# Optimization experiments

Measured on AMD Instinct MI355X. Metric: run time of the kernel, lower is better.

Reference implementation:

```python
import jax, jax.numpy as jnp
import numpy as np

B, DIN, D = 1000, 1024, 512
C, L = 1203, 77
N_INS, N_EX = 4, 5
K_SEL, K_TOP = 32, 5
HEADS, DH, MLP, NL = 8, 64, 2048, 4
TEMP = 50.0


def setup_inputs() -> dict:
    key = jax.random.key(0)
    ks = iter(jax.random.split(key, 64))

    def rn(shape, s=0.02):
        return jax.random.normal(next(ks), shape, dtype=jnp.float32) * s

    def layer_params(prefix):
        return {
            prefix + '_ln1_g': jnp.ones((NL, D)), prefix + '_ln1_b': jnp.zeros((NL, D)),
            prefix + '_qkv_w': rn((NL, D, 3 * D)), prefix + '_qkv_b': jnp.zeros((NL, 3 * D)),
            prefix + '_out_w': rn((NL, D, D)), prefix + '_out_b': jnp.zeros((NL, D)),
            prefix + '_ln2_g': jnp.ones((NL, D)), prefix + '_ln2_b': jnp.zeros((NL, D)),
            prefix + '_fc_w': rn((NL, D, MLP)), prefix + '_fc_b': jnp.zeros((NL, MLP)),
            prefix + '_pr_w': rn((NL, MLP, D)), prefix + '_pr_b': jnp.zeros((NL, D)),
        }

    zw = jax.random.normal(next(ks), (D, C + 1), dtype=jnp.float32)
    zw = zw / jnp.linalg.norm(zw, axis=0, keepdims=True)  # F.normalize(dim=0) as in __init__
    inp = {
        'x': jax.random.normal(next(ks), (B, DIN), dtype=jnp.float32),
        'linear_w': rn((DIN, D)), 'linear_b': jnp.zeros((D,)),
        'zs_weight': zw,
        'sample_w': rn((D, D)), 'sample_b': jnp.zeros((D,)),
        'ins_token': rn((N_INS, D), 0.1),
        'token_seq': rn((C, L, D), 0.1),
        'exemplar': rn((C, N_EX, D), 0.1),
        'eos_index': jax.random.randint(next(ks), (C,), 5, 60, dtype=jnp.int32),
    }
    inp.update(layer_params('agg'))
    inp['pos_emb'] = rn((L, D), 0.01)
    inp.update(layer_params('txt'))
    inp['lnf_g'] = jnp.ones((D,))
    inp['lnf_b'] = jnp.zeros((D,))
    inp['text_proj'] = rn((D, D))
    return inp


def layernorm(x, g, b, eps=1e-5):
    m = x.mean(-1, keepdims=True)
    v = x.var(-1, keepdims=True)
    return (x - m) * jax.lax.rsqrt(v + eps) * g + b


def quick_gelu(x):  # CLIP QuickGELU
    return x * jax.nn.sigmoid(1.702 * x)


def transformer(h, ln1g, ln1b, qkvw, qkvb, ow, ob, ln2g, ln2b, fcw, fcb, prw, prb, mask=None):
    # h: [N, S, D]; pre-LN residual attention blocks (CLIP style)
    Bn, S, _ = h.shape
    scale = np.float32(1.0 / np.sqrt(DH))
    for i in range(NL):
        a = layernorm(h, ln1g[i], ln1b[i])
        qkv = a @ qkvw[i] + qkvb[i]
        q, k, v = jnp.split(qkv, 3, axis=-1)
        q = q.reshape(Bn, S, HEADS, DH)
        k = k.reshape(Bn, S, HEADS, DH)
        v = v.reshape(Bn, S, HEADS, DH)
        s = jnp.einsum('bqhd,bkhd->bhqk', q, k) * scale
        if mask is not None:
            s = s + mask
        o = jnp.einsum('bhqk,bkhd->bqhd', jax.nn.softmax(s, axis=-1), v).reshape(Bn, S, D)
        h = h + o @ ow[i] + ob[i]
        m = layernorm(h, ln2g[i], ln2b[i])
        h = h + quick_gelu(m @ fcw[i] + fcb[i]) @ prw[i] + prb[i]
    return h


def inverse_sigmoid(x, eps=1e-5):
    x = jnp.clip(x, 0.0, 1.0)
    x1 = jnp.clip(x, eps, None)
    x2 = jnp.clip(1.0 - x, eps, None)
    return jnp.log(x1 / x2)


def reference(x, linear_w, linear_b, zs_weight, sample_w, sample_b, ins_token, token_seq,
              exemplar, eos_index,
              agg_ln1_g, agg_ln1_b, agg_qkv_w, agg_qkv_b, agg_out_w, agg_out_b,
              agg_ln2_g, agg_ln2_b, agg_fc_w, agg_fc_b, agg_pr_w, agg_pr_b,
              pos_emb, txt_ln1_g, txt_ln1_b, txt_qkv_w, txt_qkv_b, txt_out_w, txt_out_b,
              txt_ln2_g, txt_ln2_b, txt_fc_w, txt_fc_b, txt_pr_w, txt_pr_b,
              lnf_g, lnf_b, text_proj):
    # ---- base classifier ----
    h = x @ linear_w + linear_b                                        # [B, D]
    h = TEMP * h / jnp.linalg.norm(h, axis=1, keepdims=True)
    logits = h @ zs_weight                                             # [B, C+1]
    # ---- entropy-based proposal selection (eval path, k=32) ----
    p = jax.nn.sigmoid(logits)
    entropy = (-p * jax.nn.log_sigmoid(logits)).sum(-1)                # [B]
    _, select_index = jax.lax.top_k(entropy, K_SEL)                    # [32]
    sel_logits = logits[select_index]                                  # [32, C+1]
    _, topk_index = jax.lax.top_k(sel_logits[:, :-1], K_TOP)           # [32, 5]
    sampled_x = jax.lax.stop_gradient(h[select_index]) @ sample_w + sample_b  # [32, D]
    # ---- batched aggregator input (replaces per-proposal python loop) ----
    base = ins_token[None] + (sampled_x / TEMP)[:, None, :]            # [32, N_INS, D]
    base = jnp.broadcast_to(base[:, None], (K_SEL, K_TOP, N_INS, D))
    ex = exemplar[topk_index]                                          # [32, 5, N_EX, D]
    agg_in = jnp.concatenate([base, ex], axis=2).reshape(K_SEL * K_TOP, N_INS + N_EX, D)
    agg_out = transformer(agg_in, agg_ln1_g, agg_ln1_b, agg_qkv_w, agg_qkv_b, agg_out_w,
                          agg_out_b, agg_ln2_g, agg_ln2_b, agg_fc_w, agg_fc_b, agg_pr_w, agg_pr_b)
    ins_tokens = agg_out[:, :N_INS].reshape(K_SEL, K_TOP, N_INS, D)
    # ---- splice instance tokens into class prompts ----
    prompt = token_seq[topk_index]                                     # [32, 5, L, D]
    upd = jnp.concatenate([prompt[:, :, :2], ins_tokens, prompt[:, :, 2:L - N_INS]], axis=2)
    # ---- CLIP text encoder on updated prompts ----
    t = upd.reshape(K_SEL * K_TOP, L, D) + pos_emb
    causal = jnp.where(jnp.tril(jnp.ones((L, L), bool)), 0.0, -1e9).astype(jnp.float32)
    t = transformer(t, txt_ln1_g, txt_ln1_b, txt_qkv_w, txt_qkv_b, txt_out_w, txt_out_b,
                    txt_ln2_g, txt_ln2_b, txt_fc_w, txt_fc_b, txt_pr_w, txt_pr_b, mask=causal)
    t = layernorm(t, lnf_g, lnf_b)
    eos = (eos_index[topk_index] + 2 * N_INS).reshape(-1)              # [160]
    feats = t[jnp.arange(K_SEL * K_TOP), eos] @ text_proj              # [160, D]
    feats = feats / jnp.linalg.norm(feats, axis=-1, keepdims=True)
    rerank_logits = jnp.einsum('sd,skd->sk', sampled_x, feats.reshape(K_SEL, K_TOP, D))
    # ---- fuse + scatter back ----
    sel_det = jax.lax.stop_gradient(sel_logits)
    sel_topk = jnp.take_along_axis(sel_det, topk_index, axis=1)
    fused = jax.nn.sigmoid(sel_topk) ** 0.75 * jax.nn.sigmoid(rerank_logits) ** 0.25
    reranked = inverse_sigmoid(fused)
    rows = jnp.arange(K_SEL)[:, None]
    logits_clone = sel_det.at[rows, topk_index].set(reranked)
    logits_final = logits.at[select_index].set(logits_clone)
    return logits, rerank_logits, select_index, logits_final
```

## Files before the change

kernel.cpp:

```cpp
#include <hip/hip_runtime.h>
#include <math.h>

#define TID ((int)threadIdx.x)

constexpr int Bsz = 1000, DIN = 1024, Dm = 512, C1 = 1204, C0 = 1203, Ltok = 77;
constexpr int NINS = 4, NEX = 5, KSEL = 32, KTOP = 5, NHEAD = 8, DH = 64, MLPD = 2048, NL = 4, Pn = 160;
constexpr float TEMPc = 50.0f;

typedef __attribute__((ext_vector_type(8))) short short8;
typedef __attribute__((ext_vector_type(4))) float f32x4;
typedef __attribute__((address_space(1))) const void g1void;
typedef __attribute__((address_space(3))) void l3void;
#define GLOAD16(g, l) __builtin_amdgcn_global_load_lds((g1void*)(g), (l3void*)(l), 16, 0, 0)

__device__ __forceinline__ float sigf(float z) {
  return z >= 0.f ? 1.f / (1.f + expf(-z)) : expf(z) / (1.f + expf(z));
}

__device__ __forceinline__ float qgelu(float v) {
  return v * __fdividef(1.f, 1.f + __expf(-1.702f * v));
}

__device__ __forceinline__ unsigned short f2bfu(float f) {
  unsigned u = __builtin_bit_cast(unsigned, f);
  u += 0x7fffu + ((u >> 16) & 1u);
  return (unsigned short)(u >> 16);
}
__device__ __forceinline__ short f2bf(float f) { return (short)f2bfu(f); }

__device__ __forceinline__ void epi_store(f32x4 v, const float* bias, int colb, size_t off,
                                          int mode, float* Cf, short* Cb, float* Xres) {
  if (bias) {
    float4 bv = *(const float4*)(bias + colb);
    v[0] += bv.x; v[1] += bv.y; v[2] += bv.z; v[3] += bv.w;
  }
  if (mode == 0) {
    *(float4*)(Cf + off) = make_float4(v[0], v[1], v[2], v[3]);
  } else if (mode == 1) {
    float4* p = (float4*)(Xres + off);
    float4 o = *p;
    o.x += v[0]; o.y += v[1]; o.z += v[2]; o.w += v[3];
    *p = o;
  } else {
    if (mode == 2) {
      v[0] = qgelu(v[0]); v[1] = qgelu(v[1]); v[2] = qgelu(v[2]); v[3] = qgelu(v[3]);
    }
    uint2 pk;
    pk.x = (unsigned)f2bfu(v[0]) | ((unsigned)f2bfu(v[1]) << 16);
    pk.y = (unsigned)f2bfu(v[2]) | ((unsigned)f2bfu(v[3]) << 16);
    *(uint2*)(Cb + off) = pk;
  }
}

__global__ __launch_bounds__(256, 4) void bgemm_k(const short* __restrict__ A,
                                                  const short* __restrict__ Bt,
                                                  const float* __restrict__ bias,
                                                  float* __restrict__ Cf,
                                                  short* __restrict__ Cb,
                                                  float* __restrict__ Xres,
                                                  int M, int N, int K, int mode) {
  __shared__ short As[8192];
  __shared__ short Bs[8192];
  int nwg = gridDim.x * gridDim.y;
  int orig = blockIdx.y * gridDim.x + blockIdx.x;
  int xcd = orig & 7, lid = orig >> 3;
  int q = nwg >> 3, r = nwg & 7;
  int swz = (xcd < r ? xcd * (q + 1) : r * (q + 1) + (xcd - r) * q) + lid;
  int row0 = (swz / gridDim.x) * 128, col0 = (swz % gridDim.x) * 128;
  int lane = TID & 63;
  int w = TID >> 6;
  int wr = (TID >> 7) & 1, wc = (TID >> 6) & 1;
  int skb = (TID >> 4) & 3, si = TID & 15;
  f32x4 acc[4][4] = {};
  int nt = K >> 6;
  int kb = lane >> 4, i = lane & 15;
  for (int t = 0; t < nt; ++t) {
#pragma unroll
    for (int s = 0; s < 2; ++s) {
#pragma unroll
      for (int c = 0; c < 2; ++c) {
        int row = (c * 4 + w) * 16 + si;
        int k0 = (t << 6) + (s << 5) + skb * 8;
        GLOAD16(A + (size_t)(row0 + row) * K + k0, As + s * 4096 + (c * 256 + w * 64) * 8);
        GLOAD16(Bt + (size_t)(col0 + row) * K + k0, Bs + s * 4096 + (c * 256 + w * 64) * 8);
      }
    }
    __syncthreads();
#pragma unroll
    for (int s = 0; s < 2; ++s) {
      const short* Ab = As + s * 4096;
      const short* Bb = Bs + s * 4096;
      short8 af[4], bfr[4];
#pragma unroll
      for (int m = 0; m < 4; ++m)
        af[m] = *(const short8*)(Ab + ((((wr * 4 + m) * 4 + kb) * 16 + i) * 8));
#pragma unroll
      for (int n = 0; n < 4; ++n)
        bfr[n] = *(const short8*)(Bb + ((((wc * 4 + n) * 4 + kb) * 16 + i) * 8));
#pragma unroll
      for (int m = 0; m < 4; ++m)
#pragma unroll
        for (int n = 0; n < 4; ++n)
          acc[m][n] = __builtin_amdgcn_mfma_f32_16x16x32_bf16(bfr[n], af[m], acc[m][n], 0, 0, 0);
    }
    __syncthreads();
  }
  int li = lane & 15, lg = lane >> 4;
#pragma unroll
  for (int m = 0; m < 4; ++m) {
    int row = row0 + wr * 64 + m * 16 + li;
    if (row >= M) continue;
#pragma unroll
    for (int n = 0; n < 4; ++n) {
      int colb = col0 + wc * 64 + n * 16 + lg * 4;
      epi_store(acc[m][n], bias, colb, (size_t)row * N + colb, mode, Cf, Cb, Xres);
    }
  }
}

__global__ __launch_bounds__(512, 4) void bgemm_tall_k(const short* __restrict__ A,
                                                       const short* __restrict__ Bt,
                                                       const float* __restrict__ bias,
                                                       float* __restrict__ Cf,
                                                       short* __restrict__ Cb,
                                                       float* __restrict__ Xres,
                                                       int M, int N, int K, int mode) {
  __shared__ short As[16384];
  __shared__ short Bs[8192];
  int nwg = gridDim.x * gridDim.y;
  int orig = blockIdx.y * gridDim.x + blockIdx.x;
  int xcd = orig & 7, lid = orig >> 3;
  int q = nwg >> 3, r = nwg & 7;
  int swz = (xcd < r ? xcd * (q + 1) : r * (q + 1) + (xcd - r) * q) + lid;
  int row0 = (swz / gridDim.x) * 256, col0 = (swz % gridDim.x) * 128;
  int lane = TID & 63;
  int w = TID >> 6;
  int wr = w >> 1, wc = w & 1;
  f32x4 acc[4][4] = {};
  int nt = K >> 6;
  int kb = lane >> 4, i = lane & 15;
  int sg0 = TID >> 6, skb = (TID >> 4) & 3, si = TID & 15;
  for (int t = 0; t < nt; ++t) {
#pragma unroll
    for (int s = 0; s < 2; ++s) {
      int k0 = (t << 6) + (s << 5) + skb * 8;
#pragma unroll
      for (int c0 = 0; c0 < 2; ++c0) {
        int row = (c0 * 8 + sg0) * 16 + si;
        GLOAD16(A + (size_t)(row0 + row) * K + k0, As + s * 8192 + (c0 * 512 + TID) * 8);
      }
      {
        int row = sg0 * 16 + si;
        GLOAD16(Bt + (size_t)(col0 + row) * K + k0, Bs + s * 4096 + TID * 8);
      }
    }
    __syncthreads();
#pragma unroll
    for (int s = 0; s < 2; ++s) {
      const short* Ab = As + s * 8192;
      const short* Bb = Bs + s * 4096;
      short8 af[4], bfr[4];
#pragma unroll
      for (int m = 0; m < 4; ++m)
        af[m] = *(const short8*)(Ab + ((((wr * 4 + m) * 4 + kb) * 16 + i) * 8));
#pragma unroll
      for (int n = 0; n < 4; ++n)
        bfr[n] = *(const short8*)(Bb + ((((wc * 4 + n) * 4 + kb) * 16 + i) * 8));
#pragma unroll
      for (int m = 0; m < 4; ++m)
#pragma unroll
        for (int n = 0; n < 4; ++n)
          acc[m][n] = __builtin_amdgcn_mfma_f32_16x16x32_bf16(bfr[n], af[m], acc[m][n], 0, 0, 0);
    }
    __syncthreads();
  }
  int li = lane & 15, lg = lane >> 4;
#pragma unroll
  for (int m = 0; m < 4; ++m) {
    int row = row0 + wr * 64 + m * 16 + li;
    if (row >= M) continue;
#pragma unroll
    for (int n = 0; n < 4; ++n) {
      int colb = col0 + wc * 64 + n * 16 + lg * 4;
      epi_store(acc[m][n], bias, colb, (size_t)row * N + colb, mode, Cf, Cb, Xres);
    }
  }
}

__global__ __launch_bounds__(256) void wconv_k(const float* __restrict__ W,
                                               short* __restrict__ Wt, int K, int N) {
  int l = blockIdx.z;
  const float* Wl = W + (size_t)l * K * N;
  short* Wtl = Wt + (size_t)l * K * N;
  __shared__ float t[32][33];
  int n0 = blockIdx.x * 32, k0 = blockIdx.y * 32;
  int tx = TID & 31, ty = TID >> 5;
#pragma unroll
  for (int u = 0; u < 4; ++u)
    t[ty + u * 8][tx] = Wl[(size_t)(k0 + ty + u * 8) * N + n0 + tx];
  __syncthreads();
#pragma unroll
  for (int u = 0; u < 4; ++u)
    Wtl[(size_t)(n0 + ty + u * 8) * K + k0 + tx] = f2bf(t[tx][ty + u * 8]);
}

__global__ __launch_bounds__(256) void gemm32s_k(const float* __restrict__ A,
                                                 const float* __restrict__ W,
                                                 float* __restrict__ P,
                                                 int M, int N, int K, int KC) {
  __shared__ float As[64][17];
  __shared__ float Ws[16][65];
  int tx = TID & 15, ty = TID >> 4;
  int row0 = blockIdx.y * 64, col0 = blockIdx.x * 64;
  int kbeg = blockIdx.z * KC;
  int kend = kbeg + KC < K ? kbeg + KC : K;
  float acc[4][4] = {};
  for (int k0 = kbeg; k0 < kend; k0 += 16) {
    {
      int r = TID >> 2, c4 = (TID & 3) * 4;
      int gr = row0 + r;
#pragma unroll
      for (int u = 0; u < 4; ++u) {
        int gc = k0 + c4 + u;
        As[r][c4 + u] = (gr < M && gc < K) ? A[gr * K + gc] : 0.f;
      }
    }
    {
      int c = TID & 63;
      int gc = col0 + c;
#pragma unroll
      for (int u = 0; u < 4; ++u) {
        int rr = (TID >> 6) * 4 + u;
        int gk = k0 + rr;
        Ws[rr][c] = (gk < K && gc < N) ? W[gk * N + gc] : 0.f;
      }
    }
    __syncthreads();
#pragma unroll
    for (int kk = 0; kk < 16; ++kk) {
      float a[4], b[4];
#pragma unroll
      for (int i = 0; i < 4; ++i) a[i] = As[ty * 4 + i][kk];
#pragma unroll
      for (int j = 0; j < 4; ++j) b[j] = Ws[kk][tx * 4 + j];
#pragma unroll
      for (int i = 0; i < 4; ++i)
#pragma unroll
        for (int j = 0; j < 4; ++j) acc[i][j] += a[i] * b[j];
    }
    __syncthreads();
  }
  float* Ps = P + (size_t)blockIdx.z * M * N;
#pragma unroll
  for (int i = 0; i < 4; ++i) {
    int rrow = row0 + ty * 4 + i;
    if (rrow >= M) continue;
#pragma unroll
    for (int j = 0; j < 4; ++j) {
      int ccol = col0 + tx * 4 + j;
      if (ccol >= N) continue;
      Ps[(size_t)rrow * N + ccol] = acc[i][j];
    }
  }
}

__global__ __launch_bounds__(256) void reduce_k(const float* __restrict__ P,
                                                const float* __restrict__ bias,
                                                float* __restrict__ C,
                                                float* __restrict__ C2,
                                                int MN, int N, int S) {
  int i = blockIdx.x * 256 + TID;
  if (i >= MN) return;
  float v = 0.f;
  for (int s = 0; s < S; ++s) v += P[(size_t)s * MN + i];
  if (bias) v += bias[i % N];
  C[i] = v;
  if (C2) C2[i] = v;
}

__global__ __launch_bounds__(256) void rownorm_k(float* __restrict__ h) {
  int r = blockIdx.x;
  float* x = h + r * Dm;
  float v0 = x[TID], v1 = x[TID + 256];
  __shared__ float s1[256];
  s1[TID] = v0 * v0 + v1 * v1;
  __syncthreads();
  for (int s = 128; s; s >>= 1) { if (TID < s) s1[TID] += s1[TID + s]; __syncthreads(); }
  float sc = TEMPc / sqrtf(s1[0]);
  x[TID] = v0 * sc;
  x[TID + 256] = v1 * sc;
}

__global__ __launch_bounds__(256) void entropy_k(const float* __restrict__ logits,
                                                 double* __restrict__ ent) {
  int r = blockIdx.x;
  double acc = 0.0;
  for (int c = TID; c < C1; c += 256) {
    float z = logits[r * C1 + c];
    float ls = z >= 0.f ? -log1pf(expf(-z)) : z - log1pf(expf(z));
    float p = z >= 0.f ? 1.f / (1.f + expf(-z)) : expf(z) / (1.f + expf(z));
    acc += (double)(-p * ls);
  }
  __shared__ double sd[256];
  sd[TID] = acc;
  __syncthreads();
  for (int s = 128; s; s >>= 1) { if (TID < s) sd[TID] += sd[TID + s]; __syncthreads(); }
  if (TID == 0) ent[r] = sd[0];
}

__global__ __launch_bounds__(256) void top32_k(const double* __restrict__ ent,
                                               int* __restrict__ selidx,
                                               float* __restrict__ out2) {
  __shared__ double v[1000];
  __shared__ double wv[4];
  __shared__ int wi[4];
  for (int i = TID; i < 1000; i += 256) v[i] = ent[i];
  __syncthreads();
  int w = TID >> 6, lane = TID & 63;
  for (int r = 0; r < KSEL; ++r) {
    double bv = -1e300; int bi = 1 << 30;
    for (int i = TID; i < 1000; i += 256) {
      double x = v[i];
      if (x > bv || (x == bv && i < bi)) { bv = x; bi = i; }
    }
#pragma unroll
    for (int off = 32; off; off >>= 1) {
      double ov = __shfl_xor(bv, off, 64);
      int oi = __shfl_xor(bi, off, 64);
      if (ov > bv || (ov == bv && oi < bi)) { bv = ov; bi = oi; }
    }
    if (lane == 0) { wv[w] = bv; wi[w] = bi; }
    __syncthreads();
    if (TID == 0) {
      double fv = wv[0]; int fi = wi[0];
#pragma unroll
      for (int u = 1; u < 4; ++u)
        if (wv[u] > fv || (wv[u] == fv && wi[u] < fi)) { fv = wv[u]; fi = wi[u]; }
      selidx[r] = fi; out2[r] = (float)fi; v[fi] = -1e300;
    }
    __syncthreads();
  }
}

__global__ __launch_bounds__(256) void top5_k(const float* __restrict__ logits,
                                              const int* __restrict__ selidx,
                                              int* __restrict__ topk) {
  int s = blockIdx.x;
  int row = selidx[s];
  __shared__ float v[C0];
  __shared__ float wv[4];
  __shared__ int wi[4];
  for (int i = TID; i < C0; i += 256) v[i] = logits[row * C1 + i];
  __syncthreads();
  int w = TID >> 6, lane = TID & 63;
  for (int r = 0; r < KTOP; ++r) {
    float bv = -INFINITY; int bi = 1 << 30;
    for (int i = TID; i < C0; i += 256) {
      float x = v[i];
      if (x > bv || (x == bv && i < bi)) { bv = x; bi = i; }
    }
#pragma unroll
    for (int off = 32; off; off >>= 1) {
      float ov = __shfl_xor(bv, off, 64);
      int oi = __shfl_xor(bi, off, 64);
      if (ov > bv || (ov == bv && oi < bi)) { bv = ov; bi = oi; }
    }
    if (lane == 0) { wv[w] = bv; wi[w] = bi; }
    __syncthreads();
    if (TID == 0) {
      float fv = wv[0]; int fi = wi[0];
#pragma unroll
      for (int u = 1; u < 4; ++u)
        if (wv[u] > fv || (wv[u] == fv && wi[u] < fi)) { fv = wv[u]; fi = wi[u]; }
      topk[s * KTOP + r] = fi; v[fi] = -INFINITY;
    }
    __syncthreads();
  }
}

__global__ void eos_k(const int* __restrict__ eos_index, const int* __restrict__ topk,
                      int* __restrict__ eosl) {
  for (int p = TID; p < Pn; p += 256) eosl[p] = eos_index[topk[p]] + 2 * NINS;
}

__global__ void gather_h_k(const float* __restrict__ h, const int* __restrict__ selidx,
                           float* __restrict__ hsel) {
  int s = blockIdx.x;
  int row = selidx[s];
  for (int d = TID; d < Dm; d += 256) hsel[s * Dm + d] = h[row * Dm + d];
}

__global__ __launch_bounds__(256) void build_agg_k(const float* __restrict__ ins,
                                                   const float* __restrict__ sampled,
                                                   const float* __restrict__ ex,
                                                   const int* __restrict__ topk,
                                                   float* __restrict__ X) {
  int b = blockIdx.x;
  int p = b / 9, tok = b % 9;
  int s = p / KTOP;
#pragma unroll
  for (int u = 0; u < 2; ++u) {
    int d = TID + u * 256;
    float v;
    if (tok < NINS) v = ins[tok * Dm + d] + sampled[s * Dm + d] * (1.f / TEMPc);
    else {
      int cls = topk[p];
      v = ex[(cls * NEX + (tok - NINS)) * Dm + d];
    }
    X[b * Dm + d] = v;
  }
}

__global__ void save_ins_k(const float* __restrict__ X, float* __restrict__ insbuf) {
  int p = blockIdx.x;
  for (int i = TID; i < NINS * Dm; i += 256) insbuf[p * NINS * Dm + i] = X[p * 9 * Dm + i];
}

__global__ __launch_bounds__(256) void build_txt_k(const float* __restrict__ token_seq,
                                                   const float* __restrict__ insbuf,
                                                   const float* __restrict__ pos,
                                                   const int* __restrict__ topk,
                                                   float* __restrict__ X, int p0) {
  int b = blockIdx.x;
  int pl = b / Ltok, tok = b % Ltok;
  int p = p0 + pl;
  int cls = topk[p];
#pragma unroll
  for (int u = 0; u < 2; ++u) {
    int d = TID + u * 256;
    float v;
    if (tok < 2) v = token_seq[(cls * Ltok + tok) * Dm + d];
    else if (tok < 2 + NINS) v = insbuf[(p * NINS + (tok - 2)) * Dm + d];
    else v = token_seq[(cls * Ltok + (tok - NINS)) * Dm + d];
    X[b * Dm + d] = v + pos[tok * Dm + d];
  }
}

__global__ __launch_bounds__(256) void ln_k(const float* __restrict__ X,
                                            const float* __restrict__ g,
                                            const float* __restrict__ b,
                                            short* __restrict__ A) {
  int t = blockIdx.x;
  const float* x = X + t * Dm;
  float v0 = x[TID], v1 = x[TID + 256];
  __shared__ float s1[256], s2[256];
  s1[TID] = v0 + v1;
  s2[TID] = v0 * v0 + v1 * v1;
  __syncthreads();
  for (int s = 128; s; s >>= 1) {
    if (TID < s) { s1[TID] += s1[TID + s]; s2[TID] += s2[TID + s]; }
    __syncthreads();
  }
  float mean = s1[0] * (1.f / 512.f);
  float var = s2[0] * (1.f / 512.f) - mean * mean;
  float inv = rsqrtf(var + 1e-5f);
  A[t * Dm + TID] = f2bf((v0 - mean) * inv * g[TID] + b[TID]);
  A[t * Dm + TID + 256] = f2bf((v1 - mean) * inv * g[TID + 256] + b[TID + 256]);
}

__global__ __launch_bounds__(320) void attn_tx_k(const short* __restrict__ qkv,
                                                 short* __restrict__ O, int S) {
  __shared__ short Kf[5120];
  __shared__ short Vt[6144];
  __shared__ short Pf[5][1536];
  int p = blockIdx.x >> 3, h = blockIdx.x & 7;
  int base = p * S;
  for (int c = TID; c < 640; c += 320) {
    int i = c & 15, kb = (c >> 4) & 7, g = c >> 7;
    int j = g * 16 + i;
    short8 v = {};
    if (j < S) v = *(const short8*)(qkv + (size_t)(base + j) * 1536 + 512 + h * 64 + kb * 8);
    *(short8*)(Kf + c * 8) = v;
  }
  for (int c = TID; c < 640; c += 320) {
    int j = c >> 3;
    int d0 = (c & 7) * 8;
    short8 v = {};
    if (j < S) v = *(const short8*)(qkv + (size_t)(base + j) * 1536 + 1024 + h * 64 + d0);
    int kb = j >> 3, jj = j & 7;
#pragma unroll
    for (int u = 0; u < 8; ++u) {
      int d = d0 + u;
      Vt[(((d >> 4) * 12 + kb) * 16 + (d & 15)) * 8 + jj] = v[u];
    }
  }
  for (int c = TID; c < 128; c += 320) {
    int i = c & 15, kb = 10 + ((c >> 4) & 1), g = c >> 5;
    *(short8*)(Vt + ((g * 12 + kb) * 16 + i) * 8) = short8{};
  }
  __syncthreads();
  int w = TID >> 6, lane = TID & 63;
  int li = lane & 15, lg = lane >> 4;
  short8 aq[2];
#pragma unroll
  for (int ks = 0; ks < 2; ++ks)
    aq[ks] = *(const short8*)(qkv + (size_t)(base + w * 16 + li) * 1536 + h * 64 + ks * 32 + lg * 8);
  f32x4 accs[5] = {};
#pragma unroll
  for (int t = 0; t < 5; ++t)
#pragma unroll
    for (int ks = 0; ks < 2; ++ks) {
      short8 bk = *(const short8*)(Kf + ((t * 8 + ks * 4 + lg) * 16 + li) * 8);
      accs[t] = __builtin_amdgcn_mfma_f32_16x16x32_bf16(aq[ks], bk, accs[t], 0, 0, 0);
    }
  int rowg = w * 16 + lg * 4;
#pragma unroll
  for (int r = 0; r < 4; ++r) {
    int row = rowg + r;
    float v[5];
    float mx = -1e30f;
#pragma unroll
    for (int t = 0; t < 5; ++t) {
      int col = t * 16 + li;
      float x = accs[t][r] * 0.125f;
      bool ok = (col < S) && (col <= row);
      v[t] = ok ? x : -1e30f;
      mx = fmaxf(mx, v[t]);
    }
#pragma unroll
    for (int off = 1; off < 16; off <<= 1) mx = fmaxf(mx, __shfl_xor(mx, off, 64));
    float sum = 0.f;
#pragma unroll
    for (int t = 0; t < 5; ++t) {
      v[t] = (v[t] > -1e29f) ? __expf(v[t] - mx) : 0.f;
      sum += v[t];
    }
#pragma unroll
    for (int off = 1; off < 16; off <<= 1) sum += __shfl_xor(sum, off, 64);
    float inv = __fdividef(1.f, sum);
#pragma unroll
    for (int t = 0; t < 5; ++t) {
      int c = t * 16 + li;
      Pf[w][((c >> 3) * 16 + (row - w * 16)) * 8 + (c & 7)] = f2bf(v[t] * inv);
    }
  }
  for (int z = lane; z < 256; z += 64) {
    int kb = 10 + (z >> 7);
    int rem = z & 127;
    Pf[w][(kb * 16 + (rem >> 3)) * 8 + (rem & 7)] = 0;
  }
  f32x4 acco[4] = {};
#pragma unroll
  for (int s = 0; s < 3; ++s) {
    short8 ap = *(const short8*)(Pf[w] + ((s * 4 + lg) * 16 + li) * 8);
#pragma unroll
    for (int n = 0; n < 4; ++n) {
      short8 bv = *(const short8*)(Vt + ((n * 12 + s * 4 + lg) * 16 + li) * 8);
      acco[n] = __builtin_amdgcn_mfma_f32_16x16x32_bf16(ap, bv, acco[n], 0, 0, 0);
    }
  }
#pragma unroll
  for (int n = 0; n < 4; ++n)
#pragma unroll
    for (int r = 0; r < 4; ++r) {
      int row = rowg + r;
      if (row < S) O[(size_t)(base + row) * 512 + h * 64 + n * 16 + li] = f2bf(acco[n][r]);
    }
}

__global__ __launch_bounds__(256) void attn_k(const float* __restrict__ qkv,
                                              short* __restrict__ O, int S, int causal) {
  int blk = blockIdx.x;
  int p = blk >> 3, h = blk & 7;
  __shared__ float Qs[Ltok][68], Ks[Ltok][68], Vs[Ltok][68];
  __shared__ float ps[4][132];
  int base = p * S;
  for (int idx = TID; idx < S * 16; idx += 256) {
    int j = idx >> 4, c = idx & 15;
    const float4* q = (const float4*)(qkv + (size_t)(base + j) * 1536 + h * 64);
    const float4* k = (const float4*)(qkv + (size_t)(base + j) * 1536 + 512 + h * 64);
    const float4* v = (const float4*)(qkv + (size_t)(base + j) * 1536 + 1024 + h * 64);
    ((float4*)&Qs[j][0])[c] = q[c];
    ((float4*)&Ks[j][0])[c] = k[c];
    ((float4*)&Vs[j][0])[c] = v[c];
  }
  __syncthreads();
  int wave = TID >> 6, lane = TID & 63;
  bool val0 = lane < S, val1 = lane + 64 < S;
  int j0 = val0 ? lane : 0;
  int j1 = val1 ? lane + 64 : 0;
  const float4* k0p = (const float4*)&Ks[j0][0];
  const float4* k1p = (const float4*)&Ks[j1][0];
  for (int i = wave; i < S; i += 4) {
    const float4* q4 = (const float4*)&Qs[i][0];
    float a0 = 0.f, a1 = 0.f;
#pragma unroll
    for (int d4 = 0; d4 < 16; ++d4) {
      float4 qv = q4[d4], k0v = k0p[d4], k1v = k1p[d4];
      a0 += qv.x * k0v.x + qv.y * k0v.y + qv.z * k0v.z + qv.w * k0v.w;
      a1 += qv.x * k1v.x + qv.y * k1v.y + qv.z * k1v.z + qv.w * k1v.w;
    }
    float m0 = (val0 && (!causal || lane <= i)) ? a0 * 0.125f : -1e30f;
    float m1 = (val1 && (!causal || lane + 64 <= i)) ? a1 * 0.125f : -1e30f;
    float mx = fmaxf(m0, m1);
#pragma unroll
    for (int off = 32; off; off >>= 1) mx = fmaxf(mx, __shfl_xor(mx, off, 64));
    float e0 = expf(m0 - mx), e1 = expf(m1 - mx);
    float sum = e0 + e1;
#pragma unroll
    for (int off = 32; off; off >>= 1) sum += __shfl_xor(sum, off, 64);
    float inv = 1.f / sum;
    ps[wave][lane] = e0 * inv;
    ps[wave][lane + 64] = e1 * inv;
    float o = 0.f;
    for (int j = 0; j < S; ++j) o += ps[wave][j] * Vs[j][lane];
    O[(base + i) * Dm + h * 64 + lane] = f2bf(o);
  }
}

__global__ __launch_bounds__(256) void feats_k(const float* __restrict__ X,
                                               const int* __restrict__ eosl,
                                               const float* __restrict__ g,
                                               const float* __restrict__ bb,
                                               const float* __restrict__ proj,
                                               float* __restrict__ feats, int p0) {
  int pl = blockIdx.x;
  int p = p0 + pl;
  int e = eosl[p];
  const float* x = X + (size_t)(pl * Ltok + e) * Dm;
  __shared__ float row[Dm];
  __shared__ float s1[256], s2[256];
  float v0 = x[TID], v1 = x[TID + 256];
  s1[TID] = v0 + v1;
  s2[TID] = v0 * v0 + v1 * v1;
  __syncthreads();
  for (int s = 128; s; s >>= 1) {
    if (TID < s) { s1[TID] += s1[TID + s]; s2[TID] += s2[TID + s]; }
    __syncthreads();
  }
  float mean = s1[0] * (1.f / 512.f);
  float var = s2[0] * (1.f / 512.f) - mean * mean;
  float inv = rsqrtf(var + 1e-5f);
  row[TID] = (v0 - mean) * inv * g[TID] + bb[TID];
  row[TID + 256] = (v1 - mean) * inv * g[TID + 256] + bb[TID + 256];
  __syncthreads();
  float a0 = 0.f, a1 = 0.f;
  for (int d = 0; d < Dm; ++d) {
    float r = row[d];
    a0 += r * proj[d * Dm + TID];
    a1 += r * proj[d * Dm + TID + 256];
  }
  s1[TID] = a0 * a0 + a1 * a1;
  __syncthreads();
  for (int s = 128; s; s >>= 1) { if (TID < s) s1[TID] += s1[TID + s]; __syncthreads(); }
  float sc = 1.f / sqrtf(s1[0]);
  feats[p * Dm + TID] = a0 * sc;
  feats[p * Dm + TID + 256] = a1 * sc;
}

__global__ void rerank_k(const float* __restrict__ sampled, const float* __restrict__ feats,
                         const int* __restrict__ selidx, const int* __restrict__ topk,
                         const float* __restrict__ logits, float* __restrict__ out1,
                         float* __restrict__ out3) {
  int idx = blockIdx.x;
  int s = idx / KTOP;
  int lane = TID;
  float acc = 0.f;
  for (int d = lane; d < Dm; d += 64) acc += sampled[s * Dm + d] * feats[idx * Dm + d];
#pragma unroll
  for (int off = 32; off; off >>= 1) acc += __shfl_down(acc, off, 64);
  if (lane == 0) {
    out1[idx] = acc;
    int row = selidx[s];
    int cls = topk[idx];
    float sl = logits[row * C1 + cls];
    float a = sigf(sl), b = sigf(acc);
    float fused = powf(a, 0.75f) * powf(b, 0.25f);
    float xx = fminf(fmaxf(fused, 0.f), 1.f);
    float x1 = fmaxf(xx, 1e-5f);
    float x2 = fmaxf(1.f - xx, 1e-5f);
    out3[row * C1 + cls] = logf(x1 / x2);
  }
}

static inline size_t alup(size_t x) { return (x + 255) & ~(size_t)255; }

constexpr size_t WT_QKV = (size_t)NL * Dm * 3 * Dm;
constexpr size_t WT_OUT = (size_t)NL * Dm * Dm;
constexpr size_t WT_FC  = (size_t)NL * Dm * MLPD;
constexpr size_t WT_PR  = (size_t)NL * MLPD * Dm;
constexpr size_t WT_ALL = WT_QKV + WT_OUT + WT_FC + WT_PR;

static void plan_rows(int PC, size_t* rows_o, size_t* RP_o) {
  size_t rows = (size_t)PC * Ltok;
  if (rows < (size_t)(Pn * 9)) rows = Pn * 9;
  size_t RP = (rows + 255) & ~(size_t)255;
  *rows_o = rows; *RP_o = RP;
}

static size_t plan_bytes(int PC) {
  size_t rows, RP;
  plan_rows(PC, &rows, &RP);
  size_t tot = 0;
  tot += alup(Bsz * Dm * 4);
  tot += alup(Bsz * 8);
  tot += alup(KSEL * 4);
  tot += alup(Pn * 4);
  tot += alup(Pn * 4);
  tot += alup(KSEL * Dm * 4);
  tot += alup(KSEL * Dm * 4);
  tot += alup(Pn * NINS * Dm * 4);
  tot += alup(Pn * Dm * 4);
  tot += alup(rows * Dm * 4);
  tot += alup(RP * Dm * 2);
  tot += alup(RP * Dm * 2);
  tot += alup((size_t)(Pn * 9) * 3 * Dm * 4);
  tot += alup(RP * 3 * Dm * 2);
  tot += alup(RP * MLPD * 2);
  tot += 2 * alup(WT_ALL * 2);
  tot += alup((size_t)8 * Bsz * Dm * 4);
  tot += alup((size_t)4 * Bsz * C1 * 4);
  tot += alup((size_t)8 * KSEL * Dm * 4);
  return tot;
}

extern "C" void kernel_launch(void* const* d_in, const int* in_sizes, int n_in,
                              void* d_out, int out_size, void* d_ws, size_t ws_size,
                              hipStream_t stream) {
  const float* x         = (const float*)d_in[0];
  const float* linear_w  = (const float*)d_in[1];
  const float* linear_b  = (const float*)d_in[2];
  const float* zs_w      = (const float*)d_in[3];
  const float* sample_w  = (const float*)d_in[4];
  const float* sample_b  = (const float*)d_in[5];
  const float* ins_token = (const float*)d_in[6];
  const float* token_seq = (const float*)d_in[7];
  const float* exemplar  = (const float*)d_in[8];
  const int*   eos_index = (const int*)d_in[9];
  const float* agg_ln1_g = (const float*)d_in[10];
  const float* agg_ln1_b = (const float*)d_in[11];
  const float* agg_qkv_w = (const float*)d_in[12];
  const float* agg_qkv_b = (const float*)d_in[13];
  const float* agg_out_w = (const float*)d_in[14];
  const float* agg_out_b = (const float*)d_in[15];
  const float* agg_ln2_g = (const float*)d_in[16];
  const float* agg_ln2_b = (const float*)d_in[17];
  const float* agg_fc_w  = (const float*)d_in[18];
  const float* agg_fc_b  = (const float*)d_in[19];
  const float* agg_pr_w  = (const float*)d_in[20];
  const float* agg_pr_b  = (const float*)d_in[21];
  const float* pos_emb   = (const float*)d_in[22];
  const float* txt_ln1_g = (const float*)d_in[23];
  const float* txt_ln1_b = (const float*)d_in[24];
  const float* txt_qkv_w = (const float*)d_in[25];
  const float* txt_qkv_b = (const float*)d_in[26];
  const float* txt_out_w = (const float*)d_in[27];
  const float* txt_out_b = (const float*)d_in[28];
  const float* txt_ln2_g = (const float*)d_in[29];
  const float* txt_ln2_b = (const float*)d_in[30];
  const float* txt_fc_w  = (const float*)d_in[31];
  const float* txt_fc_b  = (const float*)d_in[32];
  const float* txt_pr_w  = (const float*)d_in[33];
  const float* txt_pr_b  = (const float*)d_in[34];
  const float* lnf_g     = (const float*)d_in[35];
  const float* lnf_b     = (const float*)d_in[36];
  const float* text_proj = (const float*)d_in[37];

  float* out0 = (float*)d_out;
  float* out1 = out0 + Bsz * C1;
  float* out2 = out1 + KSEL * KTOP;
  float* out3 = out2 + KSEL;

  int PC = 20;
  const int cands[4] = {160, 80, 40, 20};
  for (int i = 0; i < 4; ++i)
    if (plan_bytes(cands[i]) <= ws_size) { PC = cands[i]; break; }
  int NC = Pn / PC;

  char* wp = (char*)d_ws;
  auto carve = [&](size_t bytes) -> void* { void* r = (void*)wp; wp += alup(bytes); return r; };
  size_t rows, RP;
  plan_rows(PC, &rows, &RP);

  float* h       = (float*)carve(Bsz * Dm * 4);
  double* ent    = (double*)carve(Bsz * 8);
  int* selidx    = (int*)carve(KSEL * 4);
  int* topk      = (int*)carve(Pn * 4);
  int* eosl      = (int*)carve(Pn * 4);
  float* hsel    = (float*)carve(KSEL * Dm * 4);
  float* sampled = (float*)carve(KSEL * Dm * 4);
  float* insbuf  = (float*)carve(Pn * NINS * Dm * 4);
  float* feats   = (float*)carve(Pn * Dm * 4);
  float* X       = (float*)carve(rows * Dm * 4);
  short* Abuf    = (short*)carve(RP * Dm * 2);
  short* Obuf    = (short*)carve(RP * Dm * 2);
  float* QKV     = (float*)carve((size_t)(Pn * 9) * 3 * Dm * 4);
  short* QKVb    = (short*)carve(RP * 3 * Dm * 2);
  short* Hb      = (short*)carve(RP * MLPD * 2);
  short* wtA     = (short*)carve(WT_ALL * 2);
  short* wtT     = (short*)carve(WT_ALL * 2);
  float* Plin    = (float*)carve((size_t)8 * Bsz * Dm * 4);
  float* Pzs     = (float*)carve((size_t)4 * Bsz * C1 * 4);
  float* Psmp    = (float*)carve((size_t)8 * KSEL * Dm * 4);

  short* wtA_qkv = wtA;
  short* wtA_out = wtA_qkv + WT_QKV;
  short* wtA_fc  = wtA_out + WT_OUT;
  short* wtA_pr  = wtA_fc + WT_FC;
  short* wtT_qkv = wtT;
  short* wtT_out = wtT_qkv + WT_QKV;
  short* wtT_fc  = wtT_out + WT_OUT;
  short* wtT_pr  = wtT_fc + WT_FC;

  dim3 blk(256);
  auto wconv = [&](const float* W, short* Wt, int K, int N) {
    dim3 g(N / 32, K / 32, NL);
    wconv_k<<<g, blk, 0, stream>>>(W, Wt, K, N);
  };
  auto bgemm = [&](const short* A, const short* Wt, const float* bias, float* Cf, short* Cb,
                   float* Xres, int M, int N, int K, int mode) {
    if (M >= 2048 && N >= 1536) {
      dim3 g(N / 128, (M + 255) / 256);
      bgemm_tall_k<<<g, dim3(512), 0, stream>>>(A, Wt, bias, Cf, Cb, Xres, M, N, K, mode);
    } else {
      dim3 g(N / 128, (M + 127) / 128);
      bgemm_k<<<g, blk, 0, stream>>>(A, Wt, bias, Cf, Cb, Xres, M, N, K, mode);
    }
  };
  auto gemm32s = [&](const float* A, const float* W, float* P, int M, int N, int K, int S) {
    dim3 g((N + 63) / 64, (M + 63) / 64, S);
    gemm32s_k<<<g, blk, 0, stream>>>(A, W, P, M, N, K, K / S);
  };
  auto reduce = [&](const float* P, const float* bias, float* C, float* C2, int MN, int N, int S) {
    reduce_k<<<(MN + 255) / 256, blk, 0, stream>>>(P, bias, C, C2, MN, N, S);
  };

  wconv(agg_qkv_w, wtA_qkv, Dm, 3 * Dm);
  wconv(agg_out_w, wtA_out, Dm, Dm);
  wconv(agg_fc_w,  wtA_fc,  Dm, MLPD);
  wconv(agg_pr_w,  wtA_pr,  MLPD, Dm);
  wconv(txt_qkv_w, wtT_qkv, Dm, 3 * Dm);
  wconv(txt_out_w, wtT_out, Dm, Dm);
  wconv(txt_fc_w,  wtT_fc,  Dm, MLPD);
  wconv(txt_pr_w,  wtT_pr,  MLPD, Dm);

  gemm32s(x, linear_w, Plin, Bsz, Dm, DIN, 8);
  reduce(Plin, linear_b, h, nullptr, Bsz * Dm, Dm, 8);
  rownorm_k<<<Bsz, blk, 0, stream>>>(h);
  gemm32s(h, zs_w, Pzs, Bsz, C1, Dm, 4);
  reduce(Pzs, nullptr, out0, out3, Bsz * C1, C1, 4);
  entropy_k<<<Bsz, blk, 0, stream>>>(out0, ent);
  top32_k<<<1, blk, 0, stream>>>(ent, selidx, out2);
  top5_k<<<KSEL, blk, 0, stream>>>(out0, selidx, topk);
  eos_k<<<1, blk, 0, stream>>>(eos_index, topk, eosl);
  gather_h_k<<<KSEL, blk, 0, stream>>>(h, selidx, hsel);
  gemm32s(hsel, sample_w, Psmp, KSEL, Dm, Dm, 8);
  reduce(Psmp, sample_b, sampled, nullptr, KSEL * Dm, Dm, 8);

  build_agg_k<<<Pn * 9, blk, 0, stream>>>(ins_token, sampled, exemplar, topk, X);
  {
    int M = Pn * 9;
    for (int i = 0; i < NL; ++i) {
      ln_k<<<M, blk, 0, stream>>>(X, agg_ln1_g + i * Dm, agg_ln1_b + i * Dm, Abuf);
      bgemm(Abuf, wtA_qkv + (size_t)i * Dm * 3 * Dm, agg_qkv_b + i * 3 * Dm, QKV, nullptr, nullptr, M, 3 * Dm, Dm, 0);
      attn_k<<<Pn * NHEAD, blk, 0, stream>>>(QKV, Obuf, 9, 0);
      bgemm(Obuf, wtA_out + (size_t)i * Dm * Dm, agg_out_b + i * Dm, nullptr, nullptr, X, M, Dm, Dm, 1);
      ln_k<<<M, blk, 0, stream>>>(X, agg_ln2_g + i * Dm, agg_ln2_b + i * Dm, Abuf);
      bgemm(Abuf, wtA_fc + (size_t)i * Dm * MLPD, agg_fc_b + i * MLPD, nullptr, Hb, nullptr, M, MLPD, Dm, 2);
      bgemm(Hb, wtA_pr + (size_t)i * MLPD * Dm, agg_pr_b + i * Dm, nullptr, nullptr, X, M, Dm, MLPD, 1);
    }
  }
  save_ins_k<<<Pn, blk, 0, stream>>>(X, insbuf);

  for (int c = 0; c < NC; ++c) {
    int p0 = c * PC;
    int M = PC * Ltok;
    build_txt_k<<<PC * Ltok, blk, 0, stream>>>(token_seq, insbuf, pos_emb, topk, X, p0);
    for (int i = 0; i < NL; ++i) {
      ln_k<<<M, blk, 0, stream>>>(X, txt_ln1_g + i * Dm, txt_ln1_b + i * Dm, Abuf);
      bgemm(Abuf, wtT_qkv + (size_t)i * Dm * 3 * Dm, txt_qkv_b + i * 3 * Dm, nullptr, QKVb, nullptr, M, 3 * Dm, Dm, 3);
      attn_tx_k<<<dim3(PC * NHEAD), dim3(320), 0, stream>>>(QKVb, Obuf, Ltok);
      bgemm(Obuf, wtT_out + (size_t)i * Dm * Dm, txt_out_b + i * Dm, nullptr, nullptr, X, M, Dm, Dm, 1);
      ln_k<<<M, blk, 0, stream>>>(X, txt_ln2_g + i * Dm, txt_ln2_b + i * Dm, Abuf);
      bgemm(Abuf, wtT_fc + (size_t)i * Dm * MLPD, txt_fc_b + i * MLPD, nullptr, Hb, nullptr, M, MLPD, Dm, 2);
      bgemm(Hb, wtT_pr + (size_t)i * MLPD * Dm, txt_pr_b + i * Dm, nullptr, nullptr, X, M, Dm, MLPD, 1);
    }
    feats_k<<<PC, blk, 0, stream>>>(X, eosl, lnf_g, lnf_b, text_proj, feats, p0);
  }

  rerank_k<<<Pn, dim3(64), 0, stream>>>(sampled, feats, selidx, topk, out0, out1, out3);
}
```

Measured before the change: 1.972 ms.

## Split-K the aggregator residual GEMMs and use a warp-shuffle two-rows-per-block LayerNorm

Adds a split-K bf16 MFMA GEMM with an XCD-aware block swizzle. It writes partial sums, and a separate reduce kernel adds bias and the residual. It is used for the aggregator's out-projection and MLP down-projection, where M=1440 and N=512 give only 60 output tiles. The LayerNorm kernel is rewritten to handle two rows per block with float4 loads, wave shuffles and packed bf16 stores, cutting barrier-heavy tree reductions. Split-K adds extra partial-buffer traffic and an extra launch per GEMM.

New measurement: 1.812 ms (median of 2 runs). 8.1% less time.

```diff
diff --git a/kernel.cpp b/kernel.cpp
--- a/kernel.cpp
+++ b/kernel.cpp
@@ -187,6 +187,82 @@
   }
 }
 
+__global__ __launch_bounds__(256, 4) void bgemm_sk_k(const short* __restrict__ A,
+                                                     const short* __restrict__ Bt,
+                                                     float* __restrict__ P,
+                                                     int M, int N, int K, int KC) {
+  __shared__ short As[8192];
+  __shared__ short Bs[8192];
+  int nwg = gridDim.x * gridDim.y;
+  int orig = blockIdx.y * gridDim.x + blockIdx.x;
+  int xcd = orig & 7, lid = orig >> 3;
+  int q = nwg >> 3, r = nwg & 7;
+  int swz = (xcd < r ? xcd * (q + 1) : r * (q + 1) + (xcd - r) * q) + lid;
+  int row0 = (swz / gridDim.x) * 128, col0 = (swz % gridDim.x) * 128;
+  int kbeg = blockIdx.z * KC;
+  int lane = TID & 63;
+  int w = TID >> 6;
+  int wr = (TID >> 7) & 1, wc = (TID >> 6) & 1;
+  int skb = (TID >> 4) & 3, si = TID & 15;
+  f32x4 acc[4][4] = {};
+  int nt = KC >> 6;
+  int kb = lane >> 4, i = lane & 15;
+  for (int t = 0; t < nt; ++t) {
+#pragma unroll
+    for (int s = 0; s < 2; ++s) {
+#pragma unroll
+      for (int c = 0; c < 2; ++c) {
+        int row = (c * 4 + w) * 16 + si;
+        int k0 = kbeg + (t << 6) + (s << 5) + skb * 8;
+        GLOAD16(A + (size_t)(row0 + row) * K + k0, As + s * 4096 + (c * 256 + w * 64) * 8);
+        GLOAD16(Bt + (size_t)(col0 + row) * K + k0, Bs + s * 4096 + (c * 256 + w * 64) * 8);
+      }
+    }
+    __syncthreads();
+#pragma unroll
+    for (int s = 0; s < 2; ++s) {
+      const short* Ab = As + s * 4096;
+      const short* Bb = Bs + s * 4096;
+      short8 af[4], bfr[4];
+#pragma unroll
+      for (int m = 0; m < 4; ++m)
+        af[m] = *(const short8*)(Ab + ((((wr * 4 + m) * 4 + kb) * 16 + i) * 8));
+#pragma unroll
+      for (int n = 0; n < 4; ++n)
+        bfr[n] = *(const short8*)(Bb + ((((wc * 4 + n) * 4 + kb) * 16 + i) * 8));
+#pragma unroll
+      for (int m = 0; m < 4; ++m)
+#pragma unroll
+        for (int n = 0; n < 4; ++n)
+          acc[m][n] = __builtin_amdgcn_mfma_f32_16x16x32_bf16(bfr[n], af[m], acc[m][n], 0, 0, 0);
+    }
+    __syncthreads();
+  }
+  float* Pz = P + (size_t)blockIdx.z * M * N;
+  int li = lane & 15, lg = lane >> 4;
+#pragma unroll
+  for (int m = 0; m < 4; ++m) {
+    int row = row0 + wr * 64 + m * 16 + li;
+    if (row >= M) continue;
+#pragma unroll
+    for (int n = 0; n < 4; ++n) {
+      int colb = col0 + wc * 64 + n * 16 + lg * 4;
+      *(float4*)(Pz + (size_t)row * N + colb) = make_float4(acc[m][n][0], acc[m][n][1], acc[m][n][2], acc[m][n][3]);
+    }
+  }
+}
+
+__global__ __launch_bounds__(256) void reduce_res_k(const float* __restrict__ P,
+                                                    const float* __restrict__ bias,
+                                                    float* __restrict__ Xres,
+                                                    int MN, int N, int S) {
+  int i = blockIdx.x * 256 + TID;
+  if (i >= MN) return;
+  float v = bias[i % N];
+  for (int s = 0; s < S; ++s) v += P[(size_t)s * MN + i];
+  Xres[i] += v;
+}
+
 __global__ __launch_bounds__(256) void wconv_k(const float* __restrict__ W,
                                                short* __restrict__ Wt, int K, int N) {
   int l = blockIdx.z;
@@ -440,22 +516,35 @@
                                             const float* __restrict__ g,
                                             const float* __restrict__ b,
                                             short* __restrict__ A) {
-  int t = blockIdx.x;
-  const float* x = X + t * Dm;
-  float v0 = x[TID], v1 = x[TID + 256];
-  __shared__ float s1[256], s2[256];
-  s1[TID] = v0 + v1;
-  s2[TID] = v0 * v0 + v1 * v1;
-  __syncthreads();
-  for (int s = 128; s; s >>= 1) {
-    if (TID < s) { s1[TID] += s1[TID + s]; s2[TID] += s2[TID + s]; }
-    __syncthreads();
-  }
-  float mean = s1[0] * (1.f / 512.f);
-  float var = s2[0] * (1.f / 512.f) - mean * mean;
+  int t = blockIdx.x * 2 + (TID >> 7);
+  int l = TID & 127;
+  const float* x = X + (size_t)t * Dm;
+  float4 v = ((const float4*)x)[l];
+  float s1 = v.x + v.y + v.z + v.w;
+  float s2 = v.x * v.x + v.y * v.y + v.z * v.z + v.w * v.w;
+#pragma unroll
+  for (int off = 32; off; off >>= 1) {
+    s1 += __shfl_xor(s1, off, 64);
+    s2 += __shfl_xor(s2, off, 64);
+  }
+  __shared__ float w1[4], w2[4];
+  int w = TID >> 6;
+  if ((TID & 63) == 0) { w1[w] = s1; w2[w] = s2; }
+  __syncthreads();
+  int wb = (TID >> 7) << 1;
+  float S1 = w1[wb] + w1[wb + 1];
+  float S2 = w2[wb] + w2[wb + 1];
+  float mean = S1 * (1.f / 512.f);
+  float var = S2 * (1.f / 512.f) - mean * mean;
   float inv = rsqrtf(var + 1e-5f);
-  A[t * Dm + TID] = f2bf((v0 - mean) * inv * g[TID] + b[TID]);
-  A[t * Dm + TID + 256] = f2bf((v1 - mean) * inv * g[TID + 256] + b[TID + 256]);
+  float4 gv = ((const float4*)g)[l];
+  float4 bv = ((const float4*)b)[l];
+  uint2 pk;
+  pk.x = (unsigned)f2bfu((v.x - mean) * inv * gv.x + bv.x) |
+         ((unsigned)f2bfu((v.y - mean) * inv * gv.y + bv.y) << 16);
+  pk.y = (unsigned)f2bfu((v.z - mean) * inv * gv.z + bv.z) |
+         ((unsigned)f2bfu((v.w - mean) * inv * gv.w + bv.w) << 16);
+  *(uint2*)(A + (size_t)t * Dm + l * 4) = pk;
 }
 
 __global__ __launch_bounds__(320) void attn_tx_k(const short* __restrict__ qkv,
@@ -680,10 +769,11 @@
 constexpr size_t WT_FC  = (size_t)NL * Dm * MLPD;
 constexpr size_t WT_PR  = (size_t)NL * MLPD * Dm;
 constexpr size_t WT_ALL = WT_QKV + WT_OUT + WT_FC + WT_PR;
+constexpr size_t MAGG   = (size_t)Pn * 9;
 
 static void plan_rows(int PC, size_t* rows_o, size_t* RP_o) {
   size_t rows = (size_t)PC * Ltok;
-  if (rows < (size_t)(Pn * 9)) rows = Pn * 9;
+  if (rows < MAGG) rows = MAGG;
   size_t RP = (rows + 255) & ~(size_t)255;
   *rows_o = rows; *RP_o = RP;
 }
@@ -704,13 +794,14 @@
   tot += alup(rows * Dm * 4);
   tot += alup(RP * Dm * 2);
   tot += alup(RP * Dm * 2);
-  tot += alup((size_t)(Pn * 9) * 3 * Dm * 4);
+  tot += alup(MAGG * 3 * Dm * 4);
   tot += alup(RP * 3 * Dm * 2);
   tot += alup(RP * MLPD * 2);
   tot += 2 * alup(WT_ALL * 2);
   tot += alup((size_t)8 * Bsz * Dm * 4);
   tot += alup((size_t)4 * Bsz * C1 * 4);
   tot += alup((size_t)8 * KSEL * Dm * 4);
+  tot += alup((size_t)16 * MAGG * Dm * 4);
   return tot;
 }
 
@@ -784,7 +875,7 @@
   float* X       = (float*)carve(rows * Dm * 4);
   short* Abuf    = (short*)carve(RP * Dm * 2);
   short* Obuf    = (short*)carve(RP * Dm * 2);
-  float* QKV     = (float*)carve((size_t)(Pn * 9) * 3 * Dm * 4);
+  float* QKV     = (float*)carve(MAGG * 3 * Dm * 4);
   short* QKVb    = (short*)carve(RP * 3 * Dm * 2);
   short* Hb      = (short*)carve(RP * MLPD * 2);
   short* wtA     = (short*)carve(WT_ALL * 2);
@@ -792,6 +883,7 @@
   float* Plin    = (float*)carve((size_t)8 * Bsz * Dm * 4);
   float* Pzs     = (float*)carve((size_t)4 * Bsz * C1 * 4);
   float* Psmp    = (float*)carve((size_t)8 * KSEL * Dm * 4);
+  float* Psk     = (float*)carve((size_t)16 * MAGG * Dm * 4);
 
   short* wtA_qkv = wtA;
   short* wtA_out = wtA_qkv + WT_QKV;
@@ -817,12 +909,22 @@
       bgemm_k<<<g, blk, 0, stream>>>(A, Wt, bias, Cf, Cb, Xres, M, N, K, mode);
     }
   };
+  auto bgemm_res_sk = [&](const short* A, const short* Wt, const float* bias, float* Xres,
+                          int M, int N, int K, int S) {
+    dim3 g(N / 128, (M + 127) / 128, S);
+    bgemm_sk_k<<<g, blk, 0, stream>>>(A, Wt, Psk, M, N, K, K / S);
+    int MN = M * N;
+    reduce_res_k<<<(MN + 255) / 256, blk, 0, stream>>>(Psk, bias, Xres, MN, N, S);
+  };
   auto gemm32s = [&](const float* A, const float* W, float* P, int M, int N, int K, int S) {
     dim3 g((N + 63) / 64, (M + 63) / 64, S);
     gemm32s_k<<<g, blk, 0, stream>>>(A, W, P, M, N, K, K / S);
   };
   auto reduce = [&](const float* P, const float* bias, float* C, float* C2, int MN, int N, int S) {
     reduce_k<<<(MN + 255) / 256, blk, 0, stream>>>(P, bias, C, C2, MN, N, S);
+  };
+  auto ln = [&](const float* Xp, const float* g, const float* b, short* A, int M) {
+    ln_k<<<M / 2, blk, 0, stream>>>(Xp, g, b, A);
   };
 
   wconv(agg_qkv_w, wtA_qkv, Dm, 3 * Dm);
@@ -849,15 +951,15 @@
 
   build_agg_k<<<Pn * 9, blk, 0, stream>>>(ins_token, sampled, exemplar, topk, X);
   {
-    int M = Pn * 9;
+    int M = (int)MAGG;
     for (int i = 0; i < NL; ++i) {
-      ln_k<<<M, blk, 0, stream>>>(X, agg_ln1_g + i * Dm, agg_ln1_b + i * Dm, Abuf);
+      ln(X, agg_ln1_g + i * Dm, agg_ln1_b + i * Dm, Abuf, M);
       bgemm(Abuf, wtA_qkv + (size_t)i * Dm * 3 * Dm, agg_qkv_b + i * 3 * Dm, QKV, nullptr, nullptr, M, 3 * Dm, Dm, 0);
       attn_k<<<Pn * NHEAD, blk, 0, stream>>>(QKV, Obuf, 9, 0);
-      bgemm(Obuf, wtA_out + (size_t)i * Dm * Dm, agg_out_b + i * Dm, nullptr, nullptr, X, M, Dm, Dm, 1);
-      ln_k<<<M, blk, 0, stream>>>(X, agg_ln2_g + i * Dm, agg_ln2_b + i * Dm, Abuf);
+      bgemm_res_sk(Obuf, wtA_out + (size_t)i * Dm * Dm, agg_out_b + i * Dm, X, M, Dm, Dm, 8);
+      ln(X, agg_ln2_g + i * Dm, agg_ln2_b + i * Dm, Abuf, M);
       bgemm(Abuf, wtA_fc + (size_t)i * Dm * MLPD, agg_fc_b + i * MLPD, nullptr, Hb, nullptr, M, MLPD, Dm, 2);
-      bgemm(Hb, wtA_pr + (size_t)i * MLPD * Dm, agg_pr_b + i * Dm, nullptr, nullptr, X, M, Dm, MLPD, 1);
+      bgemm_res_sk(Hb, wtA_pr + (size_t)i * MLPD * Dm, agg_pr_b + i * Dm, X, M, Dm, MLPD, 16);
     }
   }
   save_ins_k<<<Pn, blk, 0, stream>>>(X, insbuf);
@@ -867,11 +969,11 @@
     int M = PC * Ltok;
     build_txt_k<<<PC * Ltok, blk, 0, stream>>>(token_seq, insbuf, pos_emb, topk, X, p0);
     for (int i = 0; i < NL; ++i) {
-      ln_k<<<M, blk, 0, stream>>>(X, txt_ln1_g + i * Dm, txt_ln1_b + i * Dm, Abuf);
+      ln(X, txt_ln1_g + i * Dm, txt_ln1_b + i * Dm, Abuf, M);
       bgemm(Abuf, wtT_qkv + (size_t)i * Dm * 3 * Dm, txt_qkv_b + i * 3 * Dm, nullptr, QKVb, nullptr, M, 3 * Dm, Dm, 3);
       attn_tx_k<<<dim3(PC * NHEAD), dim3(320), 0, stream>>>(QKVb, Obuf, Ltok);
       bgemm(Obuf, wtT_out + (size_t)i * Dm * Dm, txt_out_b + i * Dm, nullptr, nullptr, X, M, Dm, Dm, 1);
-      ln_k<<<M, blk, 0, stream>>>(X, txt_ln2_g + i * Dm, txt_ln2_b + i * Dm, Abuf);
+      ln(X, txt_ln2_g + i * Dm, txt_ln2_b + i * Dm, Abuf, M);
       bgemm(Abuf, wtT_fc + (size_t)i * Dm * MLPD, txt_fc_b + i * MLPD, nullptr, Hb, nullptr, M, MLPD, Dm, 2);
       bgemm(Hb, wtT_pr + (size_t)i * MLPD * Dm, txt_pr_b + i * Dm, nullptr, nullptr, X, M, Dm, MLPD, 1);
     }
```
